# Optimization experiments

Hardware: AMD Instinct MI355X
Metric: run time of the kernel (lower is better)

Reference implementation:

```python
import jax, jax.numpy as jnp
import numpy as np

B, N = 64, 4096          # trees per batch, leaves per complete binary tree
V, S = 21, 50            # amino-acid vocab, grammar-symbol vocab
E, H = 64, 128           # embed_dim, hidden_dim


def setup_inputs() -> dict:
    key = jax.random.key(0)
    ks = jax.random.split(key, 16)

    def lin_w(k, din, dout):
        return (jax.random.normal(k, (dout, din), jnp.float32) / np.sqrt(din)).astype(jnp.float32)

    tokens = jax.random.randint(ks[0], (B, N), 0, V, dtype=jnp.int32)
    symbols = jax.random.randint(ks[1], (B, N - 1), 0, S, dtype=jnp.int32)

    emb = jax.random.normal(ks[2], (V, E), jnp.float32) * 0.02
    emb = emb.at[0].set(0.0)  # padding_idx=0
    sym_emb = jax.random.normal(ks[3], (S, E), jnp.float32) * 0.02

    return {
        "tokens": tokens, "symbols": symbols,
        "emb": emb, "sym_emb": sym_emb,
        "Wp": lin_w(ks[4], E, H), "bp": jnp.zeros((H,), jnp.float32),
        "Wi": lin_w(ks[5], H, H), "bi": jnp.zeros((H,), jnp.float32),
        "Ui": lin_w(ks[6], H, H),
        "Wf": lin_w(ks[7], H, H), "bf": jnp.zeros((H,), jnp.float32),
        "Uf": lin_w(ks[8], H, H),
        "Wo": lin_w(ks[9], H, H), "bo": jnp.zeros((H,), jnp.float32),
        "Uo": lin_w(ks[10], H, H),
        "Wu": lin_w(ks[11], H, H), "bu": jnp.zeros((H,), jnp.float32),
        "Uu": lin_w(ks[12], H, H),
        "Wout": lin_w(ks[13], H, H), "bout": jnp.zeros((H,), jnp.float32),
    }


def _encode(tokens, symbols, emb, sym_emb, Wp, bp, Wi, bi, Ui, Wf, bf, Uf,
            Wo, bo, Uo, Wu, bu, Uu, Wout, bout):
    emb = emb.at[0].set(0.0)  # padding row contributes nothing (and gets no grad)

    # Leaf nodes: amino-acid embedding -> input_proj, no children.
    x = emb[tokens] @ Wp.T + bp                      # [B, N, H]
    i = jax.nn.sigmoid(x @ Wi.T + bi)
    o = jax.nn.sigmoid(x @ Wo.T + bo)
    u = jnp.tanh(x @ Wu.T + bu)
    c = i * u                                        # [B, N, H]
    h = o * jnp.tanh(c)

    # Bottom-up over levels of the complete binary tree (Child-Sum Tree-LSTM).
    off, n = 0, N
    while n > 1:
        m = n // 2
        xs = sym_emb[symbols[:, off:off + m]] @ Wp.T + bp   # [B, m, H]
        hl, hr = h[:, 0::2], h[:, 1::2]
        cl, cr = c[:, 0::2], c[:, 1::2]
        ht = hl + hr                                         # h_tilde = sum_j h_j
        gi = jax.nn.sigmoid(xs @ Wi.T + bi + ht @ Ui.T)
        go = jax.nn.sigmoid(xs @ Wo.T + bo + ht @ Uo.T)
        gu = jnp.tanh(xs @ Wu.T + bu + ht @ Uu.T)
        fx = xs @ Wf.T + bf
        fl = jax.nn.sigmoid(fx + hl @ Uf.T)                  # per-child forget gates
        fr = jax.nn.sigmoid(fx + hr @ Uf.T)
        c = gi * gu + fl * cl + fr * cr
        h = go * jnp.tanh(c)
        off += m
        n = m

    root_h = h[:, 0]                                         # [B, H]
    return root_h @ Wout.T + bout                            # output_proj


def reference(tokens, symbols, emb, sym_emb, Wp, bp, Wi, bi, Ui, Wf, bf, Uf,
              Wo, bo, Uo, Wu, bu, Uu, Wout, bout):
    return _encode(tokens, symbols, emb, sym_emb, Wp, bp, Wi, bi, Ui, Wf, bf,
                   Uf, Wo, bo, Uo, Wu, bu, Uu, Wout, bout)
```

## Files before the change

### kernel.cpp

```cpp
#include <hip/hip_runtime.h>
#include <hip/hip_bf16.h>

typedef __attribute__((ext_vector_type(8))) short short8;
typedef __attribute__((ext_vector_type(4))) float f32x4;

static constexpr int B_ = 64;
static constexpr int N_ = 4096;
static constexpr int V_ = 21;
static constexpr int S_ = 50;
static constexpr int E_ = 64;
static constexpr int H_ = 128;
static constexpr int NPAIR = V_ * V_;
static constexpr int NTAB = NPAIR * S_;

__device__ __forceinline__ float rcp_(float x) { return __builtin_amdgcn_rcpf(x); }
__device__ __forceinline__ float sigm(float x) { return rcp_(1.0f + __expf(-x)); }
__device__ __forceinline__ float tanh_(float x) {
  float a = fabsf(x);
  float e = __expf(-2.0f * a);
  float t = (1.0f - e) * rcp_(1.0f + e);
  return x < 0.0f ? -t : t;
}
__device__ __forceinline__ unsigned short f2bf(float f) {
  __hip_bfloat16 b = __float2bfloat16(f);
  return *reinterpret_cast<unsigned short*>(&b);
}
__device__ __forceinline__ float bf2f(unsigned short u) {
  return __uint_as_float(((unsigned int)u) << 16);
}

struct Gates { float cv, hv; };
__device__ __forceinline__ Gates gate_combine(float4 sx,
    float i_p, float o_p, float u_p, float fl_p, float fr_p, float cl, float cr) {
  float gi = sigm(sx.x + i_p);
  float go = sigm(sx.y + o_p);
  float gu = tanh_(sx.z + u_p);
  float fl = sigm(sx.w + fl_p);
  float fr = sigm(sx.w + fr_p);
  float cv = fmaf(gi, gu, fmaf(fl, cl, fr * cr));
  Gates g; g.cv = cv; g.hv = go * tanh_(cv);
  return g;
}

__global__ void __launch_bounds__(512) k_pre0(
    const float* __restrict__ Ui, const float* __restrict__ Uo,
    const float* __restrict__ Uu, const float* __restrict__ Uf,
    const float* __restrict__ Wi, const float* __restrict__ Wo,
    const float* __restrict__ Wu, const float* __restrict__ Wf,
    const float* __restrict__ Wp, const float* __restrict__ Wout,
    unsigned short* __restrict__ Wfrag, float* __restrict__ Wt,
    float* __restrict__ Wxt, float* __restrict__ Wpt,
    float* __restrict__ Woutt) {
  __shared__ float Tt[32][129];
  int blk = blockIdx.x, t = threadIdx.x;
  if (blk < 16) {
    int idx = blk * 512 + t;
    int L = idx & 63;
    int K = (idx >> 6) & 3;
    int T = idx >> 8;
    int n = 16 * T + (L & 15);
    int k0 = 32 * K + ((L >> 4) << 3);
    int g = n >> 7, o = n & 127;
    const float* U = (g == 0) ? Ui : (g == 1) ? Uo : (g == 2) ? Uu : Uf;
    unsigned short out[8];
    #pragma unroll
    for (int j = 0; j < 8; ++j) out[j] = f2bf(U[o * 128 + k0 + j]);
    *(int4*)(Wfrag + (size_t)idx * 8) = *(int4*)out;
  } else if (blk < 48) {
    int job = blk - 16;
    int m = job >> 2, kt = job & 3;
    int k0 = kt * 32;
    const float* M = (m == 0) ? Ui : (m == 1) ? Uo : (m == 2) ? Uu : (m == 3) ? Uf
                   : (m == 4) ? Wi : (m == 5) ? Wo : (m == 6) ? Wu : Wf;
    float* D = (m < 4) ? Wt : Wxt;
    int g = m & 3;
    #pragma unroll
    for (int pass = 0; pass < 2; ++pass) {
      int o = (t >> 3) + 64 * pass;
      int kk = 4 * (t & 7);
      float4 v = *(const float4*)(M + o * 128 + k0 + kk);
      Tt[kk][o] = v.x; Tt[kk + 1][o] = v.y; Tt[kk + 2][o] = v.z; Tt[kk + 3][o] = v.w;
    }
    __syncthreads();
    #pragma unroll
    for (int pass = 0; pass < 8; ++pass) {
      int kk = pass * 4 + (t >> 7);
      int o = t & 127;
      D[(size_t)(k0 + kk) * 512 + g * 128 + o] = Tt[kk][o];
    }
  } else if (blk == 48) {
    for (int i = t; i < E_ * H_; i += 512) {
      int e = i >> 7, o = i & 127;
      Wpt[i] = Wp[o * E_ + e];
    }
  } else {
    for (int i = t; i < H_ * H_; i += 512) {
      int k = i >> 7, o = i & 127;
      Woutt[i] = Wout[o * H_ + k];
    }
  }
}

__global__ void __launch_bounds__(512) k_pre1(
    const float* __restrict__ emb, const float* __restrict__ sym_emb,
    const float* __restrict__ Wpt, const float* __restrict__ Wxt,
    const float* __restrict__ Wt,
    const float* __restrict__ bp, const float* __restrict__ bi,
    const float* __restrict__ bo, const float* __restrict__ bu,
    const float* __restrict__ bfv,
    unsigned short* __restrict__ leaf_h8, float* __restrict__ leaf_c,
    float* __restrict__ symx, float* __restrict__ P_leaf) {
  __shared__ float x[128];
  __shared__ float zs[512];
  __shared__ float hl[128];
  int blk = blockIdx.x, t = threadIdx.x;
  if (blk < V_) {
    int v = blk;
    if (t < 128) {
      float acc = bp[t];
      if (v != 0) {
        for (int e = 0; e < E_; ++e) acc = fmaf(emb[v * E_ + e], Wpt[e * 128 + t], acc);
      }
      x[t] = acc;
    }
    __syncthreads();
    if (t < 384) {
      int g = t >> 7;
      const float* bb = (g == 0) ? bi : (g == 1) ? bo : bu;
      float z = bb[t & 127];
      for (int k = 0; k < H_; ++k) z = fmaf(x[k], Wxt[k * 512 + t], z);
      zs[t] = z;
    }
    __syncthreads();
    if (t < 128) {
      float gi = sigm(zs[t]), go = sigm(zs[128 + t]), gu = tanh_(zs[256 + t]);
      float c = gi * gu;
      leaf_c[v * H_ + t] = c;
      unsigned short hb = f2bf(go * tanh_(c));
      leaf_h8[v * H_ + t] = hb;
      hl[t] = bf2f(hb);
    }
    __syncthreads();
    {
      float z = 0.f;
      for (int k = 0; k < H_; ++k) z = fmaf(hl[k], Wt[k * 512 + t], z);
      P_leaf[(size_t)v * 512 + t] = z;
    }
  } else {
    int s = blk - V_;
    if (t < 128) {
      float acc = bp[t];
      for (int e = 0; e < E_; ++e) acc = fmaf(sym_emb[s * E_ + e], Wpt[e * 128 + t], acc);
      x[t] = acc;
    }
    __syncthreads();
    {
      int g = t >> 7;
      const float* bb = (g == 0) ? bi : (g == 1) ? bo : (g == 2) ? bu : bfv;
      float z = bb[t & 127];
      for (int k = 0; k < H_; ++k) z = fmaf(x[k], Wxt[k * 512 + t], z);
      zs[t] = z;
    }
    __syncthreads();
    if (t < 128) {
      float4 v4 = make_float4(zs[t], zs[128 + t], zs[256 + t], zs[384 + t]);
      *(float4*)(symx + (size_t)s * 512 + t * 4) = v4;
    }
  }
}

__global__ void k_tabB(const float* __restrict__ P_leaf, const float* __restrict__ symx,
                       const float* __restrict__ leaf_c,
                       const int* __restrict__ tokens, const int* __restrict__ symbols,
                       unsigned short* __restrict__ tab_h8, float* __restrict__ tab_c,
                       int* __restrict__ idx1) {
  int blk = blockIdx.x, t = threadIdx.x;
  if (blk < NTAB / 2) {
    int row = blk * 2 + (t >> 7);
    int u = t & 127;
    int p = row / S_, s = row - p * S_;
    int tl = p / V_, tr = p - tl * V_;
    const float* Pl = P_leaf + (size_t)tl * 512;
    const float* Pr = P_leaf + (size_t)tr * 512;
    float4 sx = *(const float4*)(symx + (size_t)s * 512 + u * 4);
    Gates gt = gate_combine(sx,
        Pl[u] + Pr[u], Pl[128 + u] + Pr[128 + u], Pl[256 + u] + Pr[256 + u],
        Pl[384 + u], Pr[384 + u],
        leaf_c[tl * H_ + u], leaf_c[tr * H_ + u]);
    tab_c[(size_t)row * H_ + u] = gt.cv;
    tab_h8[(size_t)row * H_ + u] = f2bf(gt.hv);
  } else {
    int g = (blk - NTAB / 2) * 256 + t;
    int b = g >> 11, j = g & 2047;
    idx1[g] = (tokens[b * N_ + 2 * j] * V_ + tokens[b * N_ + 2 * j + 1]) * S_ + symbols[b * (N_ - 1) + j];
  }
}

__global__ void __launch_bounds__(512, 4) k_lvl23(
    const unsigned short* __restrict__ Wfrag, const float* __restrict__ symx,
    const int* __restrict__ symbols, const int* __restrict__ idx1,
    const unsigned short* __restrict__ gh8, const float* __restrict__ gc,
    unsigned short* __restrict__ h_out8, float* __restrict__ c_out) {
  __shared__ __align__(16) unsigned short Ag[64][136];
  __shared__ __align__(16) unsigned short Bh[32][136];
  __shared__ float Bc[32][132];
  int t = threadIdx.x;
  int w = t >> 6, L = t & 63, q = L >> 4, cL = L & 15;
  int cc = 16 * w + cL;
  int g0 = blockIdx.x * 32;
  int b = g0 >> 10;
  int j2 = g0 & 1023;
  const int* sym_b = symbols + (size_t)b * (N_ - 1);
  const int* gix = idx1 + 2 * g0;

  #pragma unroll
  for (int i = 0; i < 2; ++i) {
    int fid = t + 512 * i;
    int row = fid >> 4, co = (fid & 15) * 8;
    *(int4*)&Ag[row][co] = *(const int4*)(gh8 + (size_t)gix[row] * H_ + co);
  }
  __syncthreads();

  const short8* wf = (const short8*)Wfrag;
  #pragma unroll
  for (int c = 0; c < 2; ++c) {
    float clp[4], crp[4];
    int spre[4];
    #pragma unroll
    for (int it = 0; it < 4; ++it) {
      int n = 16 * c + 8 * (it >> 1) + 2 * q + (it & 1);
      clp[it] = gc[(size_t)gix[2 * n] * H_ + cc];
      crp[it] = gc[(size_t)gix[2 * n + 1] * H_ + cc];
      spre[it] = sym_b[2048 + j2 + n];
    }
    f32x4 acc[2][4];
    #pragma unroll
    for (int r = 0; r < 2; ++r)
      #pragma unroll
      for (int g = 0; g < 4; ++g) acc[r][g] = (f32x4){0.f, 0.f, 0.f, 0.f};
    #pragma unroll
    for (int K = 0; K < 4; ++K) {
      short8 bfr[4];
      #pragma unroll
      for (int g = 0; g < 4; ++g) bfr[g] = wf[(size_t)((w + 8 * g) * 4 + K) * 64 + L];
      short8 a0 = *(const short8*)&Ag[32 * c + cL][K * 32 + q * 8];
      short8 a1 = *(const short8*)&Ag[32 * c + 16 + cL][K * 32 + q * 8];
      #pragma unroll
      for (int g = 0; g < 4; ++g) {
        acc[0][g] = __builtin_amdgcn_mfma_f32_16x16x32_bf16(a0, bfr[g], acc[0][g], 0, 0, 0);
        acc[1][g] = __builtin_amdgcn_mfma_f32_16x16x32_bf16(a1, bfr[g], acc[1][g], 0, 0, 0);
      }
    }
    #pragma unroll
    for (int r = 0; r < 2; ++r) {
      #pragma unroll
      for (int nd = 0; nd < 2; ++nd) {
        int it = r * 2 + nd;
        int n = 16 * c + 8 * r + 2 * q + nd;
        float4 sx = *(const float4*)(symx + (size_t)spre[it] * 512 + cc * 4);
        Gates gt = gate_combine(sx,
            acc[r][0][2 * nd] + acc[r][0][2 * nd + 1],
            acc[r][1][2 * nd] + acc[r][1][2 * nd + 1],
            acc[r][2][2 * nd] + acc[r][2][2 * nd + 1],
            acc[r][3][2 * nd], acc[r][3][2 * nd + 1], clp[it], crp[it]);
        Bc[n][cc] = gt.cv;
        Bh[n][cc] = f2bf(gt.hv);
      }
    }
  }
  __syncthreads();
  {
    int spre[4];
    #pragma unroll
    for (int it = 0; it < 4; ++it) {
      int n = 8 * (it >> 1) + 2 * q + (it & 1);
      spre[it] = sym_b[3072 + (j2 >> 1) + n];
    }
    f32x4 acc[2][4];
    #pragma unroll
    for (int r = 0; r < 2; ++r)
      #pragma unroll
      for (int g = 0; g < 4; ++g) acc[r][g] = (f32x4){0.f, 0.f, 0.f, 0.f};
    #pragma unroll
    for (int K = 0; K < 4; ++K) {
      short8 bfr[4];
      #pragma unroll
      for (int g = 0; g < 4; ++g) bfr[g] = wf[(size_t)((w + 8 * g) * 4 + K) * 64 + L];
      short8 a0 = *(const short8*)&Bh[cL][K * 32 + q * 8];
      short8 a1 = *(const short8*)&Bh[16 + cL][K * 32 + q * 8];
      #pragma unroll
      for (int g = 0; g < 4; ++g) {
        acc[0][g] = __builtin_amdgcn_mfma_f32_16x16x32_bf16(a0, bfr[g], acc[0][g], 0, 0, 0);
        acc[1][g] = __builtin_amdgcn_mfma_f32_16x16x32_bf16(a1, bfr[g], acc[1][g], 0, 0, 0);
      }
    }
    #pragma unroll
    for (int r = 0; r < 2; ++r) {
      #pragma unroll
      for (int nd = 0; nd < 2; ++nd) {
        int it = r * 2 + nd;
        int n = 8 * r + 2 * q + nd;
        int G3 = (g0 >> 1) + n;
        float4 sx = *(const float4*)(symx + (size_t)spre[it] * 512 + cc * 4);
        Gates gt = gate_combine(sx,
            acc[r][0][2 * nd] + acc[r][0][2 * nd + 1],
            acc[r][1][2 * nd] + acc[r][1][2 * nd + 1],
            acc[r][2][2 * nd] + acc[r][2][2 * nd + 1],
            acc[r][3][2 * nd], acc[r][3][2 * nd + 1],
            Bc[2 * n][cc], Bc[2 * n + 1][cc]);
        c_out[(size_t)G3 * H_ + cc] = gt.cv;
        h_out8[(size_t)G3 * H_ + cc] = f2bf(gt.hv);
      }
    }
  }
}

__global__ void __launch_bounds__(512, 2) k_mid(
    const unsigned short* __restrict__ Wfrag, const float* __restrict__ symx,
    const int* __restrict__ symbols,
    const unsigned short* __restrict__ in_h8, const float* __restrict__ in_c,
    unsigned short* __restrict__ out_h8, float* __restrict__ out_c) {
  __shared__ __align__(16) unsigned short Ah0[64][136];
  __shared__ __align__(16) unsigned short Ah1[32][136];
  __shared__ float Cs0[64][128];
  __shared__ float Cs1[32][128];
  int t = threadIdx.x;
  int w = t >> 6, L = t & 63, q = L >> 4, cL = L & 15;
  int cc = 16 * w + cL;
  int blk = blockIdx.x;
  int b = blk >> 3, sub = blk & 7;
  size_t base3 = (size_t)blk * 64;

  #pragma unroll
  for (int i = 0; i < 2; ++i) {
    int fid = t + 512 * i;
    int row = fid >> 4, co = (fid & 15) * 8;
    *(int4*)&Ah0[row][co] = *(const int4*)(in_h8 + (base3 + row) * H_ + co);
  }
  #pragma unroll
  for (int i = 0; i < 4; ++i) {
    int fid = t + 512 * i;
    int row = fid >> 5, c4 = (fid & 31) << 2;
    *(float4*)&Cs0[row][c4] = *(const float4*)(in_c + (base3 + row) * H_ + c4);
  }
  __syncthreads();

  const short8* wf = (const short8*)Wfrag;
  int R = 64;
  #pragma unroll
  for (int lev = 0; lev < 6; ++lev) {
    const int l = 4 + lev;
    const int nodes = R >> 1;
    const int jb = b * (N_ - 1) + (N_ - (N_ >> (l - 1))) + ((sub * 32) >> lev);
    unsigned short (*Ard)[136] = (lev & 1) ? Ah1 : Ah0;
    unsigned short (*Awr)[136] = (lev & 1) ? Ah0 : Ah1;
    const float* crd = (lev & 1) ? &Cs1[0][0] : &Cs0[0][0];
    float* cwr = (lev & 1) ? &Cs0[0][0] : &Cs1[0][0];
    const int nchunk = (nodes + 15) >> 4;
    for (int c = 0; c < nchunk; ++c) {
      int spre[4];
      #pragma unroll
      for (int it = 0; it < 4; ++it) {
        int n = 16 * c + 8 * (it >> 1) + 2 * q + (it & 1);
        spre[it] = (n < nodes) ? symbols[jb + n] : 0;
      }
      f32x4 acc[2][4];
      #pragma unroll
      for (int r = 0; r < 2; ++r)
        #pragma unroll
        for (int g = 0; g < 4; ++g) acc[r][g] = (f32x4){0.f, 0.f, 0.f, 0.f};
      const bool useA1 = (2 * nodes - 32 * c) > 16;
      #pragma unroll
      for (int K = 0; K < 4; ++K) {
        short8 bfr[4];
        #pragma unroll
        for (int g = 0; g < 4; ++g) bfr[g] = wf[(size_t)((w + 8 * g) * 4 + K) * 64 + L];
        short8 a0 = *(const short8*)&Ard[32 * c + cL][K * 32 + q * 8];
        #pragma unroll
        for (int g = 0; g < 4; ++g)
          acc[0][g] = __builtin_amdgcn_mfma_f32_16x16x32_bf16(a0, bfr[g], acc[0][g], 0, 0, 0);
        if (useA1) {
          short8 a1 = *(const short8*)&Ard[32 * c + 16 + cL][K * 32 + q * 8];
          #pragma unroll
          for (int g = 0; g < 4; ++g)
            acc[1][g] = __builtin_amdgcn_mfma_f32_16x16x32_bf16(a1, bfr[g], acc[1][g], 0, 0, 0);
        }
      }
      #pragma unroll
      for (int r = 0; r < 2; ++r) {
        #pragma unroll
        for (int nd = 0; nd < 2; ++nd) {
          int it = r * 2 + nd;
          int n = 16 * c + 8 * r + 2 * q + nd;
          if (n < nodes) {
            float4 sx = *(const float4*)(symx + (size_t)spre[it] * 512 + cc * 4);
            Gates gt = gate_combine(sx,
                acc[r][0][2 * nd] + acc[r][0][2 * nd + 1],
                acc[r][1][2 * nd] + acc[r][1][2 * nd + 1],
                acc[r][2][2 * nd] + acc[r][2][2 * nd + 1],
                acc[r][3][2 * nd], acc[r][3][2 * nd + 1],
                crd[(size_t)(2 * n) * 128 + cc], crd[(size_t)(2 * n + 1) * 128 + cc]);
            if (lev == 5) {
              out_c[(size_t)blk * H_ + cc] = gt.cv;
              out_h8[(size_t)blk * H_ + cc] = f2bf(gt.hv);
            } else {
              cwr[(size_t)n * 128 + cc] = gt.cv;
              Awr[n][cc] = f2bf(gt.hv);
            }
          }
        }
      }
    }
    __syncthreads();
    R >>= 1;
  }
}

__global__ void __launch_bounds__(512, 2) k_fin(
    const unsigned short* __restrict__ Wfrag, const float* __restrict__ symx,
    const int* __restrict__ symbols,
    const unsigned short* __restrict__ in_h8, const float* __restrict__ in_c,
    const float* __restrict__ Woutt, const float* __restrict__ bout,
    float* __restrict__ out) {
  __shared__ __align__(16) unsigned short Ah0[8][136];
  __shared__ __align__(16) unsigned short Ah1[4][136];
  __shared__ float Cs0[8][128];
  __shared__ float Cs1[4][128];
  __shared__ float rootv[128];
  int t = threadIdx.x;
  int w = t >> 6, L = t & 63, q = L >> 4, cL = L & 15;
  int cc = 16 * w + cL;
  int b = blockIdx.x;

  if (t < 128) {
    int row = t >> 4, co = (t & 15) * 8;
    *(int4*)&Ah0[row][co] = *(const int4*)(in_h8 + (size_t)(b * 8 + row) * H_ + co);
  }
  if (t < 256) {
    int row = t >> 5, c4 = (t & 31) << 2;
    *(float4*)&Cs0[row][c4] = *(const float4*)(in_c + (size_t)(b * 8 + row) * H_ + c4);
  }
  __syncthreads();

  const short8* wf = (const short8*)Wfrag;
  int R = 8;
  #pragma unroll
  for (int lev = 0; lev < 3; ++lev) {
    const int l = 10 + lev;
    const int nodes = R >> 1;
    const int jb = b * (N_ - 1) + (N_ - (N_ >> (l - 1)));
    unsigned short (*Ard)[136] = (lev & 1) ? Ah1 : Ah0;
    unsigned short (*Awr)[136] = (lev & 1) ? Ah0 : Ah1;
    const float* crd = (lev & 1) ? &Cs1[0][0] : &Cs0[0][0];
    float* cwr = (lev & 1) ? &Cs0[0][0] : &Cs1[0][0];
    int spre[4];
    #pragma unroll
    for (int it = 0; it < 4; ++it) {
      int n = 8 * (it >> 1) + 2 * q + (it & 1);
      spre[it] = (n < nodes) ? symbols[jb + n] : 0;
    }
    f32x4 acc[4];
    #pragma unroll
    for (int g = 0; g < 4; ++g) acc[g] = (f32x4){0.f, 0.f, 0.f, 0.f};
    #pragma unroll
    for (int K = 0; K < 4; ++K) {
      short8 bfr[4];
      #pragma unroll
      for (int g = 0; g < 4; ++g) bfr[g] = wf[(size_t)((w + 8 * g) * 4 + K) * 64 + L];
      short8 a0 = *(const short8*)&Ard[cL & 7][K * 32 + q * 8];
      #pragma unroll
      for (int g = 0; g < 4; ++g)
        acc[g] = __builtin_amdgcn_mfma_f32_16x16x32_bf16(a0, bfr[g], acc[g], 0, 0, 0);
    }
    #pragma unroll
    for (int nd = 0; nd < 2; ++nd) {
      int it = nd;
      int n = 2 * q + nd;
      if (n < nodes) {
        float4 sx = *(const float4*)(symx + (size_t)spre[it] * 512 + cc * 4);
        Gates gt = gate_combine(sx,
            acc[0][2 * nd] + acc[0][2 * nd + 1],
            acc[1][2 * nd] + acc[1][2 * nd + 1],
            acc[2][2 * nd] + acc[2][2 * nd + 1],
            acc[3][2 * nd], acc[3][2 * nd + 1],
            crd[(size_t)(2 * n) * 128 + cc], crd[(size_t)(2 * n + 1) * 128 + cc]);
        if (lev == 2) {
          rootv[cc] = gt.hv;
        } else {
          cwr[(size_t)n * 128 + cc] = gt.cv;
          Awr[n][cc] = f2bf(gt.hv);
        }
      }
    }
    __syncthreads();
    R >>= 1;
  }
  if (t < 128) {
    float acc = bout[t];
    for (int k = 0; k < H_; ++k) acc = fmaf(rootv[k], Woutt[k * 128 + t], acc);
    out[(size_t)b * H_ + t] = acc;
  }
}

extern "C" void kernel_launch(void* const* d_in, const int* in_sizes, int n_in,
                              void* d_out, int out_size, void* d_ws, size_t ws_size,
                              hipStream_t stream) {
  const int* tokens    = (const int*)d_in[0];
  const int* symbols   = (const int*)d_in[1];
  const float* emb     = (const float*)d_in[2];
  const float* sym_emb = (const float*)d_in[3];
  const float* Wp  = (const float*)d_in[4];
  const float* bp  = (const float*)d_in[5];
  const float* Wi  = (const float*)d_in[6];
  const float* bi  = (const float*)d_in[7];
  const float* Ui  = (const float*)d_in[8];
  const float* Wf  = (const float*)d_in[9];
  const float* bf  = (const float*)d_in[10];
  const float* Uf  = (const float*)d_in[11];
  const float* Wo  = (const float*)d_in[12];
  const float* bo  = (const float*)d_in[13];
  const float* Uo  = (const float*)d_in[14];
  const float* Wu  = (const float*)d_in[15];
  const float* bu  = (const float*)d_in[16];
  const float* Uu  = (const float*)d_in[17];
  const float* Wout= (const float*)d_in[18];
  const float* bout= (const float*)d_in[19];

  char* ws = (char*)d_ws;
  unsigned short* Wfrag   = (unsigned short*)(ws);
  float*          Wt      = (float*)(ws + 131072);
  float*          Wxt     = (float*)(ws + 393216);
  float*          Wpt     = (float*)(ws + 655360);
  float*          Woutt   = (float*)(ws + 688128);
  unsigned short* leaf_h8 = (unsigned short*)(ws + 753664);
  float*          leaf_c  = (float*)(ws + 759040);
  float*          symx    = (float*)(ws + 769792);
  float*          P_leaf  = (float*)(ws + 872192);
  unsigned short* tab_h8  = (unsigned short*)(ws + 2001152UL);
  float*          tab_c   = (float*)(ws + 7645952UL);
  int*            idx1    = (int*)(ws + 18935552UL);
  unsigned short* L3h8    = (unsigned short*)(ws + 19459840UL);
  float*          L3c     = (float*)(ws + 27848448UL);
  unsigned short* L9h8    = (unsigned short*)(ws + 44625664UL);
  float*          L9c     = (float*)(ws + 44756736UL);

  k_pre0<<<50, 512, 0, stream>>>(Ui, Uo, Uu, Uf, Wi, Wo, Wu, Wf, Wp, Wout,
                                 Wfrag, Wt, Wxt, Wpt, Woutt);
  k_pre1<<<V_ + S_, 512, 0, stream>>>(emb, sym_emb, Wpt, Wxt, Wt,
                                      bp, bi, bo, bu, bf,
                                      leaf_h8, leaf_c, symx, P_leaf);
  k_tabB<<<NTAB / 2 + 512, 256, 0, stream>>>(P_leaf, symx, leaf_c, tokens, symbols,
                                             tab_h8, tab_c, idx1);
  k_lvl23<<<2048, 512, 0, stream>>>(Wfrag, symx, symbols, idx1, tab_h8, tab_c, L3h8, L3c);
  k_mid<<<512, 512, 0, stream>>>(Wfrag, symx, symbols, L3h8, L3c, L9h8, L9c);
  k_fin<<<B_, 512, 0, stream>>>(Wfrag, symx, symbols, L9h8, L9c, Woutt, bout,
                                (float*)d_out);
}
```

Baseline: 216.2 us.

## Compute level-1 nodes on the fly instead of precomputing full pair table

Drops the precomputed lookup table over all (left token, right token, symbol) combinations, which held about 22k rows of h and c. The table kernel is replaced by a small kernel that packs the indices, and the level-1 gate math now runs inside k_lvl23 straight from the per-token projections. This removes writing the large table and gathering rows from it later. In exchange it repeats the transcendental gate math for each of the 128k level-1 nodes instead of once per table entry, and it needs more scattered reads of small cached arrays.

```diff
diff --git a/kernel.cpp b/kernel.cpp
--- a/kernel.cpp
+++ b/kernel.cpp
@@ -10,8 +10,6 @@
 static constexpr int S_ = 50;
 static constexpr int E_ = 64;
 static constexpr int H_ = 128;
-static constexpr int NPAIR = V_ * V_;
-static constexpr int NTAB = NPAIR * S_;
 
 __device__ __forceinline__ float rcp_(float x) { return __builtin_amdgcn_rcpf(x); }
 __device__ __forceinline__ float sigm(float x) { return rcp_(1.0f + __expf(-x)); }
@@ -169,37 +167,20 @@
   }
 }
 
-__global__ void k_tabB(const float* __restrict__ P_leaf, const float* __restrict__ symx,
-                       const float* __restrict__ leaf_c,
-                       const int* __restrict__ tokens, const int* __restrict__ symbols,
-                       unsigned short* __restrict__ tab_h8, float* __restrict__ tab_c,
-                       int* __restrict__ idx1) {
-  int blk = blockIdx.x, t = threadIdx.x;
-  if (blk < NTAB / 2) {
-    int row = blk * 2 + (t >> 7);
-    int u = t & 127;
-    int p = row / S_, s = row - p * S_;
-    int tl = p / V_, tr = p - tl * V_;
-    const float* Pl = P_leaf + (size_t)tl * 512;
-    const float* Pr = P_leaf + (size_t)tr * 512;
-    float4 sx = *(const float4*)(symx + (size_t)s * 512 + u * 4);
-    Gates gt = gate_combine(sx,
-        Pl[u] + Pr[u], Pl[128 + u] + Pr[128 + u], Pl[256 + u] + Pr[256 + u],
-        Pl[384 + u], Pr[384 + u],
-        leaf_c[tl * H_ + u], leaf_c[tr * H_ + u]);
-    tab_c[(size_t)row * H_ + u] = gt.cv;
-    tab_h8[(size_t)row * H_ + u] = f2bf(gt.hv);
-  } else {
-    int g = (blk - NTAB / 2) * 256 + t;
-    int b = g >> 11, j = g & 2047;
-    idx1[g] = (tokens[b * N_ + 2 * j] * V_ + tokens[b * N_ + 2 * j + 1]) * S_ + symbols[b * (N_ - 1) + j];
-  }
+__global__ void k_idx(const int* __restrict__ tokens, const int* __restrict__ symbols,
+                      int* __restrict__ pidx) {
+  int g = blockIdx.x * 256 + threadIdx.x;
+  int b = g >> 11, j = g & 2047;
+  int tl = tokens[b * N_ + 2 * j];
+  int tr = tokens[b * N_ + 2 * j + 1];
+  int s = symbols[b * (N_ - 1) + j];
+  pidx[g] = (tl << 16) | (tr << 8) | s;
 }
 
 __global__ void __launch_bounds__(512, 4) k_lvl23(
     const unsigned short* __restrict__ Wfrag, const float* __restrict__ symx,
-    const int* __restrict__ symbols, const int* __restrict__ idx1,
-    const unsigned short* __restrict__ gh8, const float* __restrict__ gc,
+    const int* __restrict__ symbols, const int* __restrict__ pidx,
+    const float* __restrict__ P_leaf, const float* __restrict__ leaf_c,
     unsigned short* __restrict__ h_out8, float* __restrict__ c_out) {
   __shared__ __align__(16) unsigned short Ag[64][136];
   __shared__ __align__(16) unsigned short Bh[32][136];
@@ -211,26 +192,44 @@
   int b = g0 >> 10;
   int j2 = g0 & 1023;
   const int* sym_b = symbols + (size_t)b * (N_ - 1);
-  const int* gix = idx1 + 2 * g0;
-
+  const int* pix = pidx + 2 * g0;
+
+  float creg[2][2][2][2];
   #pragma unroll
-  for (int i = 0; i < 2; ++i) {
-    int fid = t + 512 * i;
-    int row = fid >> 4, co = (fid & 15) * 8;
-    *(int4*)&Ag[row][co] = *(const int4*)(gh8 + (size_t)gix[row] * H_ + co);
+  for (int c = 0; c < 2; ++c) {
+    #pragma unroll
+    for (int r = 0; r < 2; ++r) {
+      #pragma unroll
+      for (int nd = 0; nd < 2; ++nd) {
+        #pragma unroll
+        for (int ch = 0; ch < 2; ++ch) {
+          int n = 16 * c + 8 * r + 2 * q + nd;
+          int row = 2 * n + ch;
+          int pk = pix[row];
+          int tl = pk >> 16, tr = (pk >> 8) & 255, s = pk & 255;
+          const float* Pl = P_leaf + (size_t)tl * 512;
+          const float* Pr = P_leaf + (size_t)tr * 512;
+          float4 sx = *(const float4*)(symx + (size_t)s * 512 + cc * 4);
+          Gates g1 = gate_combine(sx,
+              Pl[cc] + Pr[cc], Pl[128 + cc] + Pr[128 + cc],
+              Pl[256 + cc] + Pr[256 + cc],
+              Pl[384 + cc], Pr[384 + cc],
+              leaf_c[tl * H_ + cc], leaf_c[tr * H_ + cc]);
+          creg[c][r][nd][ch] = g1.cv;
+          Ag[row][cc] = f2bf(g1.hv);
+        }
+      }
+    }
   }
   __syncthreads();
 
   const short8* wf = (const short8*)Wfrag;
   #pragma unroll
   for (int c = 0; c < 2; ++c) {
-    float clp[4], crp[4];
     int spre[4];
     #pragma unroll
     for (int it = 0; it < 4; ++it) {
       int n = 16 * c + 8 * (it >> 1) + 2 * q + (it & 1);
-      clp[it] = gc[(size_t)gix[2 * n] * H_ + cc];
-      crp[it] = gc[(size_t)gix[2 * n + 1] * H_ + cc];
       spre[it] = sym_b[2048 + j2 + n];
     }
     f32x4 acc[2][4];
@@ -262,7 +261,8 @@
             acc[r][0][2 * nd] + acc[r][0][2 * nd + 1],
             acc[r][1][2 * nd] + acc[r][1][2 * nd + 1],
             acc[r][2][2 * nd] + acc[r][2][2 * nd + 1],
-            acc[r][3][2 * nd], acc[r][3][2 * nd + 1], clp[it], crp[it]);
+            acc[r][3][2 * nd], acc[r][3][2 * nd + 1],
+            creg[c][r][nd][0], creg[c][r][nd][1]);
         Bc[n][cc] = gt.cv;
         Bh[n][cc] = f2bf(gt.hv);
       }
@@ -453,10 +453,10 @@
     unsigned short (*Awr)[136] = (lev & 1) ? Ah0 : Ah1;
     const float* crd = (lev & 1) ? &Cs1[0][0] : &Cs0[0][0];
     float* cwr = (lev & 1) ? &Cs0[0][0] : &Cs1[0][0];
-    int spre[4];
-    #pragma unroll
-    for (int it = 0; it < 4; ++it) {
-      int n = 8 * (it >> 1) + 2 * q + (it & 1);
+    int spre[2];
+    #pragma unroll
+    for (int it = 0; it < 2; ++it) {
+      int n = 2 * q + it;
       spre[it] = (n < nodes) ? symbols[jb + n] : 0;
     }
     f32x4 acc[4];
@@ -474,10 +474,9 @@
     }
     #pragma unroll
     for (int nd = 0; nd < 2; ++nd) {
-      int it = nd;
       int n = 2 * q + nd;
       if (n < nodes) {
-        float4 sx = *(const float4*)(symx + (size_t)spre[it] * 512 + cc * 4);
+        float4 sx = *(const float4*)(symx + (size_t)spre[nd] * 512 + cc * 4);
         Gates gt = gate_combine(sx,
             acc[0][2 * nd] + acc[0][2 * nd + 1],
             acc[1][2 * nd] + acc[1][2 * nd + 1],
@@ -536,22 +535,20 @@
   float*          leaf_c  = (float*)(ws + 759040);
   float*          symx    = (float*)(ws + 769792);
   float*          P_leaf  = (float*)(ws + 872192);
-  unsigned short* tab_h8  = (unsigned short*)(ws + 2001152UL);
-  float*          tab_c   = (float*)(ws + 7645952UL);
-  int*            idx1    = (int*)(ws + 18935552UL);
-  unsigned short* L3h8    = (unsigned short*)(ws + 19459840UL);
-  float*          L3c     = (float*)(ws + 27848448UL);
-  unsigned short* L9h8    = (unsigned short*)(ws + 44625664UL);
-  float*          L9c     = (float*)(ws + 44756736UL);
+  int*            pidx    = (int*)(ws + 915200);
+  unsigned short* L3h8    = (unsigned short*)(ws + 1439488UL);
+  float*          L3c     = (float*)(ws + 9828096UL);
+  unsigned short* L9h8    = (unsigned short*)(ws + 26605312UL);
+  float*          L9c     = (float*)(ws + 26736384UL);
 
   k_pre0<<<50, 512, 0, stream>>>(Ui, Uo, Uu, Uf, Wi, Wo, Wu, Wf, Wp, Wout,
                                  Wfrag, Wt, Wxt, Wpt, Woutt);
   k_pre1<<<V_ + S_, 512, 0, stream>>>(emb, sym_emb, Wpt, Wxt, Wt,
                                       bp, bi, bo, bu, bf,
                                       leaf_h8, leaf_c, symx, P_leaf);
-  k_tabB<<<NTAB / 2 + 512, 256, 0, stream>>>(P_leaf, symx, leaf_c, tokens, symbols,
-                                             tab_h8, tab_c, idx1);
-  k_lvl23<<<2048, 512, 0, stream>>>(Wfrag, symx, symbols, idx1, tab_h8, tab_c, L3h8, L3c);
+  k_idx<<<512, 256, 0, stream>>>(tokens, symbols, pidx);
+  k_lvl23<<<2048, 512, 0, stream>>>(Wfrag, symx, symbols, pidx, P_leaf, leaf_c,
+                                    L3h8, L3c);
   k_mid<<<512, 512, 0, stream>>>(Wfrag, symx, symbols, L3h8, L3c, L9h8, L9c);
   k_fin<<<B_, 512, 0, stream>>>(Wfrag, symx, symbols, L9h8, L9c, Woutt, bout,
                                 (float*)d_out);
```

Result: slower. 241.1 us (+11.5%).
